# Optimization experiments

Hardware: AMD Instinct MI355X
Metric: run time of the kernel (lower is better)

The kernel has to match this reference:

```python
import jax, jax.numpy as jnp
import numpy as np
import math

D_MODEL = 1024
NUM_HEADS = 16
D_K = D_MODEL // NUM_HEADS


def setup_inputs() -> dict:
    key = jax.random.key(0)
    ks = jax.random.split(key, 9)
    s = 1.0 / math.sqrt(D_MODEL)
    x = jax.random.normal(ks[0], (2, 2048, D_MODEL), dtype=jnp.float32)
    # torch Linear params: weight [out, in], bias [out]
    Wq = jax.random.uniform(ks[1], (D_MODEL, D_MODEL), jnp.float32, -s, s)
    bq = jax.random.uniform(ks[2], (D_MODEL,), jnp.float32, -s, s)
    Wk = jax.random.uniform(ks[3], (D_MODEL, D_MODEL), jnp.float32, -s, s)
    bk = jax.random.uniform(ks[4], (D_MODEL,), jnp.float32, -s, s)
    Wv = jax.random.uniform(ks[5], (D_MODEL, D_MODEL), jnp.float32, -s, s)
    bv = jax.random.uniform(ks[6], (D_MODEL,), jnp.float32, -s, s)
    Wo = jax.random.uniform(ks[7], (D_MODEL, D_MODEL), jnp.float32, -s, s)
    bo = jax.random.uniform(ks[8], (D_MODEL,), jnp.float32, -s, s)
    return {"x": x, "Wq": Wq, "bq": bq, "Wk": Wk, "bk": bk,
            "Wv": Wv, "bv": bv, "Wo": Wo, "bo": bo}


def reference(x, Wq, bq, Wk, bk, Wv, bv, Wo, bo):
    B, T, _ = x.shape
    scale = 1.0 / math.sqrt(D_MODEL)  # NOTE: module scales by sqrt(d_model), not sqrt(d_k)

    def proj(W, b):
        # torch Linear: x @ W^T + b, then split heads -> [B, H, T, d_k]
        y = jnp.einsum('btd,ed->bte', x, W) + b
        return y.reshape(B, T, NUM_HEADS, D_K).transpose(0, 2, 1, 3)

    Q = proj(Wq, bq)
    K = proj(Wk, bk)
    V = proj(Wv, bv)
    logits = jnp.einsum('bhtd,bhsd->bhts', Q, K) * scale  # [B,H,T,T]
    attn = jax.nn.softmax(logits, axis=-1)
    out = jnp.einsum('bhts,bhsd->bhtd', attn, V)  # [B,H,T,d_k]
    out = out.transpose(0, 2, 1, 3).reshape(B, T, D_MODEL)
    return jnp.einsum('btd,ed->bte', out, Wo) + bo
```

## Files before the change

### kernel.cpp

```cpp
#include <hip/hip_runtime.h>

#define T_SEQ 2048
#define NB 2
#define NH 16
#define DK 64
#define DMODEL 1024

typedef __bf16 bf16x8 __attribute__((ext_vector_type(8)));
typedef float f32x4 __attribute__((ext_vector_type(4)));
typedef unsigned short ushortx8 __attribute__((ext_vector_type(8)));
typedef unsigned short ushortx4 __attribute__((ext_vector_type(4)));

__device__ inline unsigned short f2b1(float f) {
  unsigned u = __float_as_uint(f);
  u += 0x7fffu + ((u >> 16) & 1u);
  return (unsigned short)(u >> 16);
}

__device__ inline void gload16(const void* g, void* l) {
  __builtin_amdgcn_global_load_lds((const __attribute__((address_space(1))) void*)g,
                                   (__attribute__((address_space(3))) void*)l, 16, 0, 0);
}

__global__ void f2b_kernel(const float* __restrict__ src, unsigned short* __restrict__ dst, int n) {
  int i = (blockIdx.x * blockDim.x + threadIdx.x) * 4;
  if (i >= n) return;
  float4 v = *(const float4*)(src + i);
  ushortx4 o;
  o.x = f2b1(v.x); o.y = f2b1(v.y); o.z = f2b1(v.z); o.w = f2b1(v.w);
  *(ushortx4*)(dst + i) = o;
}

__global__ void f2b4(const float* __restrict__ w0, const float* __restrict__ w1,
                     const float* __restrict__ w2, const float* __restrict__ w3,
                     unsigned short* __restrict__ dst) {
  int which = blockIdx.x >> 10;
  int i = ((blockIdx.x & 1023) * 256 + threadIdx.x) * 4;
  const float* src = which == 0 ? w0 : which == 1 ? w1 : which == 2 ? w2 : w3;
  float4 v = *(const float4*)(src + i);
  ushortx4 o;
  o.x = f2b1(v.x); o.y = f2b1(v.y); o.z = f2b1(v.z); o.w = f2b1(v.w);
  *(ushortx4*)(dst + (long)which * 1048576 + i) = o;
}

__global__ void biascat(const float* __restrict__ bq, const float* __restrict__ bk,
                        const float* __restrict__ bv, float* __restrict__ out) {
  int i = blockIdx.x * blockDim.x + threadIdx.x;
  if (i >= 3072) return;
  float v = (i < 1024) ? bq[i] : (i < 2048 ? bk[i - 1024] : bv[i - 2048]);
  out[i] = v;
}

__global__ __launch_bounds__(256, 2)
void gemm_bt(const unsigned short* __restrict__ A, const unsigned short* __restrict__ B,
             const float* __restrict__ bias, unsigned short* __restrict__ Cb,
             float* __restrict__ Cf, int M, int N, int K, int scale_cols, float scl) {
  __shared__ unsigned short As[4096];
  __shared__ unsigned short Bs[4096];
  const int tid = threadIdx.x;
  const int w = tid >> 6, lane = tid & 63;
  const int quad = lane >> 4, l16 = lane & 15;
  const int bm = blockIdx.y, bn = blockIdx.x;
  const int wm = w >> 1, wn = w & 1;

  f32x4 acc[4][4] = {};

  const int srow = tid >> 2;
  const int c4 = tid & 3;
  const unsigned short* aG = A + (long)(bm * 128 + srow) * K + c4 * 8;
  const unsigned short* bG = B + (long)(bn * 128 + srow) * K + c4 * 8;
  unsigned short* asW = As + w * 512;
  unsigned short* bsW = Bs + w * 512;
  const long rs64 = (long)64 * K;

  for (int kt = 0; kt < K; kt += 32) {
    __syncthreads();
    gload16(aG + kt, asW);
    gload16(aG + rs64 + kt, asW + 2048);
    gload16(bG + kt, bsW);
    gload16(bG + rs64 + kt, bsW + 2048);
    __syncthreads();

    bf16x8 af[4], bfr[4];
#pragma unroll
    for (int mt = 0; mt < 4; mt++)
      af[mt] = *(const bf16x8*)(As + (wm * 64 + mt * 16 + l16) * 32 + quad * 8);
#pragma unroll
    for (int nt = 0; nt < 4; nt++)
      bfr[nt] = *(const bf16x8*)(Bs + (wn * 64 + nt * 16 + l16) * 32 + quad * 8);
#pragma unroll
    for (int mt = 0; mt < 4; mt++)
#pragma unroll
      for (int nt = 0; nt < 4; nt++)
        acc[mt][nt] = __builtin_amdgcn_mfma_f32_16x16x32_bf16(af[mt], bfr[nt], acc[mt][nt], 0, 0, 0);
  }

  const int col0 = bn * 128 + wn * 64 + l16;
#pragma unroll
  for (int mt = 0; mt < 4; mt++) {
    int row0 = bm * 128 + wm * 64 + mt * 16 + quad * 4;
#pragma unroll
    for (int nt = 0; nt < 4; nt++) {
      int col = col0 + nt * 16;
      float bb = bias[col];
      float s = (col < scale_cols) ? scl : 1.0f;
#pragma unroll
      for (int r = 0; r < 4; r++) {
        float v = (acc[mt][nt][r] + bb) * s;
        if (Cf) Cf[(long)(row0 + r) * N + col] = v;
        else    Cb[(long)(row0 + r) * N + col] = f2b1(v);
      }
    }
  }
}

__global__ __launch_bounds__(256)
void vtrans(const unsigned short* __restrict__ QKV, unsigned short* __restrict__ Vt) {
  __shared__ unsigned short tile[64 * 80];
  int tid = threadIdx.x;
  int b = blockIdx.y >> 4, h = blockIdx.y & 15, tt = blockIdx.x;
  const unsigned short* base = QKV + (long)(b * T_SEQ + tt * 64) * 3072 + 2048 + h * 64;
#pragma unroll
  for (int rr = 0; rr < 2; rr++) {
    int L = rr * 256 + tid;
    int row = L >> 3, c = L & 7;
    ushortx8 v = *(const ushortx8*)(base + (long)row * 3072 + c * 8);
    *(ushortx8*)(tile + row * 80 + c * 8) = v;
  }
  __syncthreads();
  unsigned short* obase = Vt + (long)((b * NH + h) * DK) * T_SEQ + tt * 64;
#pragma unroll
  for (int rr = 0; rr < 2; rr++) {
    int L = rr * 256 + tid;
    int d = L >> 3, c = L & 7;
    ushortx8 o;
#pragma unroll
    for (int j = 0; j < 8; j++) o[j] = tile[(c * 8 + j) * 80 + d];
    *(ushortx8*)(obase + (long)d * T_SEQ + c * 8) = o;
  }
}

__global__ __launch_bounds__(256)
void attn2(const unsigned short* __restrict__ QKV, const unsigned short* __restrict__ Vt,
           float* __restrict__ Onum, float* __restrict__ Oden) {
  __shared__ unsigned short Ks[4096];
  __shared__ unsigned short Vs[4096];
  __shared__ unsigned short Ps[4 * 2304];
  const int tid = threadIdx.x;
  const int w = tid >> 6, lane = tid & 63;
  const int quad = lane >> 4, l16 = lane & 15;

  const int id = blockIdx.x;
  const int group = (id & 7) | (((id >> 3) & 7) << 3);
  const int qt = id >> 6;
  const int bh = group >> 1, split = group & 1;
  const int b = bh >> 4, h = bh & 15;
  const long qkvBase = (long)b * T_SEQ * 3072;
  const int kv0 = split * 1024;

  bf16x8 qf[2][2];
#pragma unroll
  for (int g = 0; g < 2; g++) {
    const unsigned short* qp = QKV + qkvBase + (long)(qt * 128 + w * 32 + g * 16 + l16) * 3072 + h * 64 + quad * 8;
    qf[g][0] = *(const bf16x8*)qp;
    qf[g][1] = *(const bf16x8*)(qp + 32);
  }

  const unsigned short* kG[2];
  const unsigned short* vG[2];
#pragma unroll
  for (int i = 0; i < 2; i++) {
    int S = w * 128 + i * 64 + lane;
    int krow = S >> 3;
    int kc = (S & 7) ^ ((krow >> 2) & 7);
    kG[i] = QKV + qkvBase + 1024 + h * 64 + (long)(kv0 + krow) * 3072 + kc * 8;
    int drow = S >> 3;
    int vc = (S & 7) ^ (drow & 7);
    vG[i] = Vt + (long)bh * DK * T_SEQ + (long)drow * T_SEQ + kv0 + vc * 8;
  }
  char* ksW = (char*)Ks + w * 2048;
  char* vsW = (char*)Vs + w * 2048;
  unsigned short* psW = Ps + w * 2304;

  f32x4 acco[2][4] = {};
  float psum[2][4] = {};

  for (int it = 0; it < 16; it++) {
    __syncthreads();
    gload16(kG[0], ksW);
    gload16(kG[1], ksW + 1024);
    gload16(vG[0], vsW);
    gload16(vG[1], vsW + 1024);
    kG[0] += 64 * 3072; kG[1] += 64 * 3072;
    vG[0] += 64;        vG[1] += 64;
    __syncthreads();

    const int sw = (l16 & 7) * 16;
    f32x4 s[2][4];
#pragma unroll
    for (int nt = 0; nt < 4; nt++) {
      const char* kb = (char*)Ks + (4 * l16 + nt) * 128;
      bf16x8 k0 = *(const bf16x8*)(kb + ((quad * 16) ^ sw));
      bf16x8 k1 = *(const bf16x8*)(kb + ((64 + quad * 16) ^ sw));
#pragma unroll
      for (int g = 0; g < 2; g++) {
        f32x4 z = {};
        z = __builtin_amdgcn_mfma_f32_16x16x32_bf16(qf[g][0], k0, z, 0, 0, 0);
        z = __builtin_amdgcn_mfma_f32_16x16x32_bf16(qf[g][1], k1, z, 0, 0, 0);
        s[g][nt] = z;
      }
    }

#pragma unroll
    for (int g = 0; g < 2; g++)
#pragma unroll
      for (int r = 0; r < 4; r++) {
        float p0 = __builtin_amdgcn_exp2f(s[g][0][r]);
        float p1 = __builtin_amdgcn_exp2f(s[g][1][r]);
        float p2 = __builtin_amdgcn_exp2f(s[g][2][r]);
        float p3 = __builtin_amdgcn_exp2f(s[g][3][r]);
        psum[g][r] += (p0 + p1) + (p2 + p3);
        unsigned a0 = __float_as_uint(p0) + 0x8000u;
        unsigned a1 = __float_as_uint(p1) + 0x8000u;
        unsigned a2 = __float_as_uint(p2) + 0x8000u;
        unsigned a3 = __float_as_uint(p3) + 0x8000u;
        uint2 pk;
        pk.x = __builtin_amdgcn_perm(a1, a0, 0x07060302u);
        pk.y = __builtin_amdgcn_perm(a3, a2, 0x07060302u);
        *(uint2*)(psW + (g * 16 + quad * 4 + r) * 72 + l16 * 4) = pk;
      }

    bf16x8 pa[2][2];
#pragma unroll
    for (int g = 0; g < 2; g++) {
      pa[g][0] = *(const bf16x8*)(psW + (g * 16 + l16) * 72 + quad * 8);
      pa[g][1] = *(const bf16x8*)(psW + (g * 16 + l16) * 72 + 32 + quad * 8);
    }

#pragma unroll
    for (int nt = 0; nt < 4; nt++) {
      const char* vb = (char*)Vs + (nt * 16 + l16) * 128;
      bf16x8 v0 = *(const bf16x8*)(vb + ((quad * 16) ^ sw));
      bf16x8 v1 = *(const bf16x8*)(vb + ((64 + quad * 16) ^ sw));
#pragma unroll
      for (int g = 0; g < 2; g++) {
        acco[g][nt] = __builtin_amdgcn_mfma_f32_16x16x32_bf16(pa[g][0], v0, acco[g][nt], 0, 0, 0);
        acco[g][nt] = __builtin_amdgcn_mfma_f32_16x16x32_bf16(pa[g][1], v1, acco[g][nt], 0, 0, 0);
      }
    }
  }

  const long rowBase = (long)bh * T_SEQ + qt * 128 + w * 32;
  const long numBase = ((long)split * 65536 + rowBase) * 64;
#pragma unroll
  for (int g = 0; g < 2; g++)
#pragma unroll
    for (int r = 0; r < 4; r++) {
      float v = psum[g][r];
      v += __shfl_xor(v, 1, 64);
      v += __shfl_xor(v, 2, 64);
      v += __shfl_xor(v, 4, 64);
      v += __shfl_xor(v, 8, 64);
      if (l16 == 0)
        Oden[(long)split * 65536 + rowBase + g * 16 + quad * 4 + r] = v;
#pragma unroll
      for (int nt = 0; nt < 4; nt++)
        Onum[numBase + (long)(g * 16 + quad * 4 + r) * 64 + nt * 16 + l16] = acco[g][nt][r];
    }
}

__global__ __launch_bounds__(256)
void combine(const float* __restrict__ Onum, const float* __restrict__ Oden,
             unsigned short* __restrict__ Ob) {
  int idx = blockIdx.x * 256 + threadIdx.x;
  int rp = idx >> 4;
  int dq = (idx & 15) * 4;
  float4 n0 = *(const float4*)(Onum + (long)rp * 64 + dq);
  float4 n1 = *(const float4*)(Onum + 4194304L + (long)rp * 64 + dq);
  float den = Oden[rp] + Oden[65536 + rp];
  float rl = __builtin_amdgcn_rcpf(den);
  int bh = rp >> 11, t = rp & 2047;
  int b = bh >> 4, h = bh & 15;
  ushortx4 o;
  o.x = f2b1((n0.x + n1.x) * rl);
  o.y = f2b1((n0.y + n1.y) * rl);
  o.z = f2b1((n0.z + n1.z) * rl);
  o.w = f2b1((n0.w + n1.w) * rl);
  *(ushortx4*)(Ob + (long)(b * T_SEQ + t) * DMODEL + h * 64 + dq) = o;
}

extern "C" void kernel_launch(void* const* d_in, const int* in_sizes, int n_in,
                              void* d_out, int out_size, void* d_ws, size_t ws_size,
                              hipStream_t stream) {
  const float* x  = (const float*)d_in[0];
  const float* Wq = (const float*)d_in[1];
  const float* bq = (const float*)d_in[2];
  const float* Wk = (const float*)d_in[3];
  const float* bk = (const float*)d_in[4];
  const float* Wv = (const float*)d_in[5];
  const float* bv = (const float*)d_in[6];
  const float* Wo = (const float*)d_in[7];
  const float* bo = (const float*)d_in[8];
  float* out = (float*)d_out;

  unsigned short* xb   = (unsigned short*)d_ws;
  unsigned short* Wqkv = xb + 4194304;
  unsigned short* Wob  = Wqkv + 3145728;
  float*          bqkv = (float*)(Wob + 1048576);
  unsigned short* QKV  = (unsigned short*)(bqkv + 3072);
  unsigned short* Vt   = QKV + 12582912;
  unsigned short* Ob   = Vt + 4194304;
  float*          Onum = (float*)(Ob + 4194304);
  float*          Oden = Onum + 8388608;

  f2b_kernel<<<4096, 256, 0, stream>>>(x, xb, 4194304);
  f2b4<<<4096, 256, 0, stream>>>(Wq, Wk, Wv, Wo, Wqkv);
  biascat<<<12, 256, 0, stream>>>(bq, bk, bv, bqkv);

  gemm_bt<<<dim3(24, 32), 256, 0, stream>>>(xb, Wqkv, bqkv, QKV, nullptr,
                                            4096, 3072, 1024, 1024, 0.04508422037f);

  vtrans<<<dim3(32, 32), 256, 0, stream>>>(QKV, Vt);
  attn2<<<dim3(1024), 256, 0, stream>>>(QKV, Vt, Onum, Oden);
  combine<<<dim3(4096), 256, 0, stream>>>(Onum, Oden, Ob);

  gemm_bt<<<dim3(8, 32), 256, 0, stream>>>(Ob, Wob, bo, nullptr, out,
                                           4096, 1024, 1024, 0, 1.0f);
}
```

Baseline: 221.3 us.

## Double-buffer LDS tiles in GEMM and attention, fuse prep kernels

Both the GEMM and the attention kernels now use two LDS buffers. The loads for the next K or KV tile are issued before computing on the current tile, so each loop iteration needs one barrier instead of two, and global-to-LDS traffic can overlap with MFMA work. The attention P scratch is halved by reusing one 16-row region per group. The three conversion and bias-concat launches are merged into a single prep kernel to save launch overhead. In exchange, LDS use per block goes up, and the final iteration prefetches one tile past the range, which is an out-of-bounds read at the buffer tail.

New measurement: 215.5 us. -2.6%, faster.

```diff
diff --git a/kernel.cpp b/kernel.cpp
--- a/kernel.cpp
+++ b/kernel.cpp
@@ -22,41 +22,43 @@
                                    (__attribute__((address_space(3))) void*)l, 16, 0, 0);
 }
 
-__global__ void f2b_kernel(const float* __restrict__ src, unsigned short* __restrict__ dst, int n) {
-  int i = (blockIdx.x * blockDim.x + threadIdx.x) * 4;
-  if (i >= n) return;
-  float4 v = *(const float4*)(src + i);
-  ushortx4 o;
-  o.x = f2b1(v.x); o.y = f2b1(v.y); o.z = f2b1(v.z); o.w = f2b1(v.w);
-  *(ushortx4*)(dst + i) = o;
-}
-
-__global__ void f2b4(const float* __restrict__ w0, const float* __restrict__ w1,
+__global__ void prep(const float* __restrict__ x,
+                     const float* __restrict__ w0, const float* __restrict__ w1,
                      const float* __restrict__ w2, const float* __restrict__ w3,
-                     unsigned short* __restrict__ dst) {
-  int which = blockIdx.x >> 10;
-  int i = ((blockIdx.x & 1023) * 256 + threadIdx.x) * 4;
-  const float* src = which == 0 ? w0 : which == 1 ? w1 : which == 2 ? w2 : w3;
-  float4 v = *(const float4*)(src + i);
-  ushortx4 o;
-  o.x = f2b1(v.x); o.y = f2b1(v.y); o.z = f2b1(v.z); o.w = f2b1(v.w);
-  *(ushortx4*)(dst + (long)which * 1048576 + i) = o;
-}
-
-__global__ void biascat(const float* __restrict__ bq, const float* __restrict__ bk,
-                        const float* __restrict__ bv, float* __restrict__ out) {
-  int i = blockIdx.x * blockDim.x + threadIdx.x;
-  if (i >= 3072) return;
-  float v = (i < 1024) ? bq[i] : (i < 2048 ? bk[i - 1024] : bv[i - 2048]);
-  out[i] = v;
+                     const float* __restrict__ bq, const float* __restrict__ bk,
+                     const float* __restrict__ bv,
+                     unsigned short* __restrict__ xb, unsigned short* __restrict__ Wqkv,
+                     float* __restrict__ bqkv) {
+  int bid = blockIdx.x, tid = threadIdx.x;
+  if (bid < 4096) {
+    int i = (bid * 256 + tid) * 4;
+    float4 v = *(const float4*)(x + i);
+    ushortx4 o;
+    o.x = f2b1(v.x); o.y = f2b1(v.y); o.z = f2b1(v.z); o.w = f2b1(v.w);
+    *(ushortx4*)(xb + i) = o;
+  } else if (bid < 8192) {
+    int which = (bid - 4096) >> 10;
+    int i = (((bid - 4096) & 1023) * 256 + tid) * 4;
+    const float* src = which == 0 ? w0 : which == 1 ? w1 : which == 2 ? w2 : w3;
+    float4 v = *(const float4*)(src + i);
+    ushortx4 o;
+    o.x = f2b1(v.x); o.y = f2b1(v.y); o.z = f2b1(v.z); o.w = f2b1(v.w);
+    *(ushortx4*)(Wqkv + (long)which * 1048576 + i) = o;
+  } else {
+    int i = (bid - 8192) * 256 + tid;
+    if (i < 3072) {
+      float v = (i < 1024) ? bq[i] : (i < 2048 ? bk[i - 1024] : bv[i - 2048]);
+      bqkv[i] = v;
+    }
+  }
 }
 
 __global__ __launch_bounds__(256, 2)
 void gemm_bt(const unsigned short* __restrict__ A, const unsigned short* __restrict__ B,
              const float* __restrict__ bias, unsigned short* __restrict__ Cb,
              float* __restrict__ Cf, int M, int N, int K, int scale_cols, float scl) {
-  __shared__ unsigned short As[4096];
-  __shared__ unsigned short Bs[4096];
+  __shared__ unsigned short As[2][4096];
+  __shared__ unsigned short Bs[2][4096];
   const int tid = threadIdx.x;
   const int w = tid >> 6, lane = tid & 63;
   const int quad = lane >> 4, l16 = lane & 15;
@@ -69,30 +71,38 @@
   const int c4 = tid & 3;
   const unsigned short* aG = A + (long)(bm * 128 + srow) * K + c4 * 8;
   const unsigned short* bG = B + (long)(bn * 128 + srow) * K + c4 * 8;
-  unsigned short* asW = As + w * 512;
-  unsigned short* bsW = Bs + w * 512;
   const long rs64 = (long)64 * K;
-
+  const int wo = w * 512;
+
+  gload16(aG, As[0] + wo);
+  gload16(aG + rs64, As[0] + 2048 + wo);
+  gload16(bG, Bs[0] + wo);
+  gload16(bG + rs64, Bs[0] + 2048 + wo);
+
+  int buf = 0;
   for (int kt = 0; kt < K; kt += 32) {
     __syncthreads();
-    gload16(aG + kt, asW);
-    gload16(aG + rs64 + kt, asW + 2048);
-    gload16(bG + kt, bsW);
-    gload16(bG + rs64 + kt, bsW + 2048);
-    __syncthreads();
+    {
+      const int nb = buf ^ 1;
+      gload16(aG + kt + 32, As[nb] + wo);
+      gload16(aG + rs64 + kt + 32, As[nb] + 2048 + wo);
+      gload16(bG + kt + 32, Bs[nb] + wo);
+      gload16(bG + rs64 + kt + 32, Bs[nb] + 2048 + wo);
+    }
 
     bf16x8 af[4], bfr[4];
 #pragma unroll
     for (int mt = 0; mt < 4; mt++)
-      af[mt] = *(const bf16x8*)(As + (wm * 64 + mt * 16 + l16) * 32 + quad * 8);
+      af[mt] = *(const bf16x8*)(As[buf] + (wm * 64 + mt * 16 + l16) * 32 + quad * 8);
 #pragma unroll
     for (int nt = 0; nt < 4; nt++)
-      bfr[nt] = *(const bf16x8*)(Bs + (wn * 64 + nt * 16 + l16) * 32 + quad * 8);
+      bfr[nt] = *(const bf16x8*)(Bs[buf] + (wn * 64 + nt * 16 + l16) * 32 + quad * 8);
 #pragma unroll
     for (int mt = 0; mt < 4; mt++)
 #pragma unroll
       for (int nt = 0; nt < 4; nt++)
         acc[mt][nt] = __builtin_amdgcn_mfma_f32_16x16x32_bf16(af[mt], bfr[nt], acc[mt][nt], 0, 0, 0);
+    buf ^= 1;
   }
 
   const int col0 = bn * 128 + wn * 64 + l16;
@@ -143,9 +153,9 @@
 __global__ __launch_bounds__(256)
 void attn2(const unsigned short* __restrict__ QKV, const unsigned short* __restrict__ Vt,
            float* __restrict__ Onum, float* __restrict__ Oden) {
-  __shared__ unsigned short Ks[4096];
-  __shared__ unsigned short Vs[4096];
-  __shared__ unsigned short Ps[4 * 2304];
+  __shared__ unsigned short Ks[2][4096];
+  __shared__ unsigned short Vs[2][4096];
+  __shared__ unsigned short Ps[4 * 1152];
   const int tid = threadIdx.x;
   const int w = tid >> 6, lane = tid & 63;
   const int quad = lane >> 4, l16 = lane & 15;
@@ -174,32 +184,40 @@
     int krow = S >> 3;
     int kc = (S & 7) ^ ((krow >> 2) & 7);
     kG[i] = QKV + qkvBase + 1024 + h * 64 + (long)(kv0 + krow) * 3072 + kc * 8;
-    int drow = S >> 3;
-    int vc = (S & 7) ^ (drow & 7);
-    vG[i] = Vt + (long)bh * DK * T_SEQ + (long)drow * T_SEQ + kv0 + vc * 8;
-  }
-  char* ksW = (char*)Ks + w * 2048;
-  char* vsW = (char*)Vs + w * 2048;
-  unsigned short* psW = Ps + w * 2304;
+    int vc = (S & 7) ^ (krow & 7);
+    vG[i] = Vt + (long)bh * DK * T_SEQ + (long)krow * T_SEQ + kv0 + vc * 8;
+  }
+  unsigned short* psW = Ps + w * 1152;
+  const int wo2 = w * 1024;
+
+  gload16(kG[0], Ks[0] + wo2);
+  gload16(kG[1], Ks[0] + wo2 + 512);
+  gload16(vG[0], Vs[0] + wo2);
+  gload16(vG[1], Vs[0] + wo2 + 512);
+  kG[0] += 64 * 3072; kG[1] += 64 * 3072;
+  vG[0] += 64;        vG[1] += 64;
 
   f32x4 acco[2][4] = {};
   float psum[2][4] = {};
+  int buf = 0;
 
   for (int it = 0; it < 16; it++) {
     __syncthreads();
-    gload16(kG[0], ksW);
-    gload16(kG[1], ksW + 1024);
-    gload16(vG[0], vsW);
-    gload16(vG[1], vsW + 1024);
-    kG[0] += 64 * 3072; kG[1] += 64 * 3072;
-    vG[0] += 64;        vG[1] += 64;
-    __syncthreads();
+    {
+      const int nb = buf ^ 1;
+      gload16(kG[0], Ks[nb] + wo2);
+      gload16(kG[1], Ks[nb] + wo2 + 512);
+      gload16(vG[0], Vs[nb] + wo2);
+      gload16(vG[1], Vs[nb] + wo2 + 512);
+      kG[0] += 64 * 3072; kG[1] += 64 * 3072;
+      vG[0] += 64;        vG[1] += 64;
+    }
 
     const int sw = (l16 & 7) * 16;
     f32x4 s[2][4];
 #pragma unroll
     for (int nt = 0; nt < 4; nt++) {
-      const char* kb = (char*)Ks + (4 * l16 + nt) * 128;
+      const char* kb = (char*)(Ks[buf]) + (4 * l16 + nt) * 128;
       bf16x8 k0 = *(const bf16x8*)(kb + ((quad * 16) ^ sw));
       bf16x8 k1 = *(const bf16x8*)(kb + ((64 + quad * 16) ^ sw));
 #pragma unroll
@@ -211,8 +229,9 @@
       }
     }
 
-#pragma unroll
-    for (int g = 0; g < 2; g++)
+    bf16x8 pa[2][2];
+#pragma unroll
+    for (int g = 0; g < 2; g++) {
 #pragma unroll
       for (int r = 0; r < 4; r++) {
         float p0 = __builtin_amdgcn_exp2f(s[g][0][r]);
@@ -227,19 +246,15 @@
         uint2 pk;
         pk.x = __builtin_amdgcn_perm(a1, a0, 0x07060302u);
         pk.y = __builtin_amdgcn_perm(a3, a2, 0x07060302u);
-        *(uint2*)(psW + (g * 16 + quad * 4 + r) * 72 + l16 * 4) = pk;
+        *(uint2*)(psW + (quad * 4 + r) * 72 + l16 * 4) = pk;
       }
-
-    bf16x8 pa[2][2];
-#pragma unroll
-    for (int g = 0; g < 2; g++) {
-      pa[g][0] = *(const bf16x8*)(psW + (g * 16 + l16) * 72 + quad * 8);
-      pa[g][1] = *(const bf16x8*)(psW + (g * 16 + l16) * 72 + 32 + quad * 8);
+      pa[g][0] = *(const bf16x8*)(psW + l16 * 72 + quad * 8);
+      pa[g][1] = *(const bf16x8*)(psW + l16 * 72 + 32 + quad * 8);
     }
 
 #pragma unroll
     for (int nt = 0; nt < 4; nt++) {
-      const char* vb = (char*)Vs + (nt * 16 + l16) * 128;
+      const char* vb = (char*)(Vs[buf]) + (nt * 16 + l16) * 128;
       bf16x8 v0 = *(const bf16x8*)(vb + ((quad * 16) ^ sw));
       bf16x8 v1 = *(const bf16x8*)(vb + ((64 + quad * 16) ^ sw));
 #pragma unroll
@@ -248,6 +263,7 @@
         acco[g][nt] = __builtin_amdgcn_mfma_f32_16x16x32_bf16(pa[g][1], v1, acco[g][nt], 0, 0, 0);
       }
     }
+    buf ^= 1;
   }
 
   const long rowBase = (long)bh * T_SEQ + qt * 128 + w * 32;
@@ -313,9 +329,7 @@
   float*          Onum = (float*)(Ob + 4194304);
   float*          Oden = Onum + 8388608;
 
-  f2b_kernel<<<4096, 256, 0, stream>>>(x, xb, 4194304);
-  f2b4<<<4096, 256, 0, stream>>>(Wq, Wk, Wv, Wo, Wqkv);
-  biascat<<<12, 256, 0, stream>>>(bq, bk, bv, bqkv);
+  prep<<<8204, 256, 0, stream>>>(x, Wq, Wk, Wv, Wo, bq, bk, bv, xb, Wqkv, bqkv);
 
   gemm_bt<<<dim3(24, 32), 256, 0, stream>>>(xb, Wqkv, bqkv, QKV, nullptr,
                                             4096, 3072, 1024, 1024, 0.04508422037f);
```
